# Optimization experiments

Measured on AMD Instinct MI355X. Metric: run time of the kernel, lower is better.

Reference implementation:

```python
import jax, jax.numpy as jnp
import numpy as np

B, L, D, H = 2, 2048, 1024, 16
HD = D // H  # head_dim = 64


def _clin(xr, xi, Wr, br, Wi, bi):
    # (x_r + i x_i)(W_r + i W_i): out_r = fc_r(x_r) - fc_i(x_i); out_i = fc_r(x_i) + fc_i(x_r)
    rr = xr @ Wr.T + br
    ii = xi @ Wi.T + bi
    ri = xi @ Wr.T + br
    ir = xr @ Wi.T + bi
    return rr - ii, ri + ir


def _heads(x):
    # [B, L, D] -> [B, H, L, HD]
    return x.reshape(B, L, H, HD).transpose(0, 2, 1, 3)


def setup_inputs() -> dict:
    key = jax.random.key(0)
    ks = jax.random.split(key, 11)
    inp = {
        "x_r": jax.random.normal(ks[0], (B, L, D), jnp.float32),
        "x_i": jax.random.normal(ks[1], (B, L, D), jnp.float32),
        "attention_mask": jnp.zeros((B, 1, 1, L), jnp.float32),
    }
    names = ["Wq_r", "Wq_i", "Wk_r", "Wk_i", "Wv_r", "Wv_i", "Wo_r", "Wo_i"]
    for n, k in zip(names, ks[2:10]):
        inp[n] = jax.random.normal(k, (D, D), jnp.float32) * 0.02
        inp["b" + n[1:]] = jnp.zeros((D,), jnp.float32)
    return inp


def reference(x_r, x_i, attention_mask,
              Wq_r, bq_r, Wq_i, bq_i,
              Wk_r, bk_r, Wk_i, bk_i,
              Wv_r, bv_r, Wv_i, bv_i,
              Wo_r, bo_r, Wo_i, bo_i):
    qr, qi = _clin(x_r, x_i, Wq_r, bq_r, Wq_i, bq_i)
    kr, ki = _clin(x_r, x_i, Wk_r, bk_r, Wk_i, bk_i)
    vr, vi = _clin(x_r, x_i, Wv_r, bv_r, Wv_i, bv_i)
    q_r, q_i = _heads(qr), _heads(qi)
    k_r, k_i = _heads(kr), _heads(ki)
    v_r, v_i = _heads(vr), _heads(vi)
    # complex QK^T cross terms -> squared-magnitude interference score
    s_real = jnp.einsum('bhqd,bhkd->bhqk', q_r, k_r) + jnp.einsum('bhqd,bhkd->bhqk', q_i, k_i)
    s_imag = jnp.einsum('bhqd,bhkd->bhqk', q_i, k_r) - jnp.einsum('bhqd,bhkd->bhqk', q_r, k_i)
    interference = (s_real * s_real + s_imag * s_imag) / HD + attention_mask
    attn = jax.nn.softmax(interference, axis=-1)
    c_r = jnp.einsum('bhqk,bhkd->bhqd', attn, v_r).transpose(0, 2, 1, 3).reshape(B, L, D)
    c_i = jnp.einsum('bhqk,bhkd->bhqd', attn, v_i).transpose(0, 2, 1, 3).reshape(B, L, D)
    out_r, out_i = _clin(c_r, c_i, Wo_r, bo_r, Wo_i, bo_i)
    return out_r, out_i
```

## Files before the change

kernel.cpp:

```cpp
#include <hip/hip_runtime.h>
#include <hip/hip_bf16.h>

typedef unsigned short u16;
typedef __attribute__((ext_vector_type(8))) short bf16x8;
typedef __attribute__((ext_vector_type(8))) _Float16 f16x8;
typedef __attribute__((ext_vector_type(8))) unsigned short u16x8;
typedef __attribute__((ext_vector_type(4))) float f32x4;

__device__ __forceinline__ u16 f2b(float f) {
  _Float16 h = (_Float16)f;
  return __builtin_bit_cast(u16, h);
}

__device__ __forceinline__ f32x4 mfma16(bf16x8 a, bf16x8 b, f32x4 c) {
  return __builtin_amdgcn_mfma_f32_16x16x32_f16(
      __builtin_bit_cast(f16x8, a), __builtin_bit_cast(f16x8, b), c, 0, 0, 0);
}

#define GLD16(dst, src) __builtin_amdgcn_global_load_lds( \
    (const __attribute__((address_space(1))) void*)(src), \
    (__attribute__((address_space(3))) void*)(dst), 16, 0, 0)

__global__ void pack_x_kernel(u16* __restrict__ A1, const float* __restrict__ xr,
                              const float* __restrict__ xi) {
  const int id = blockIdx.x * 256 + threadIdx.x;
  const size_t k8 = (size_t)id * 8;
  const int n = (int)(k8 >> 11);
  const int kk = (int)(k8 & 2047);
  const float* src = (kk < 1024) ? (xr + (size_t)n * 1024 + kk)
                                 : (xi + (size_t)n * 1024 + (kk - 1024));
  float4 a = *(const float4*)src;
  float4 c = *(const float4*)(src + 4);
  u16x8 o;
  o[0] = f2b(a.x); o[1] = f2b(a.y); o[2] = f2b(a.z); o[3] = f2b(a.w);
  o[4] = f2b(c.x); o[5] = f2b(c.y); o[6] = f2b(c.z); o[7] = f2b(c.w);
  *(u16x8*)(A1 + k8) = o;
}

__global__ void pack_w_kernel(u16* __restrict__ dst, float* __restrict__ biasDst,
                              const float* __restrict__ Wr, const float* __restrict__ Wi,
                              const float* __restrict__ br, const float* __restrict__ bi,
                              int isim) {
  const int row = blockIdx.x;
  const int kk = threadIdx.x * 8;
  const int half = kk >> 10;
  const int kloc = kk & 1023;
  const float* W = (half == 0) ? (isim ? Wi : Wr) : (isim ? Wr : Wi);
  const float sgn = (half == 1 && !isim) ? -1.f : 1.f;
  const float* src = W + (size_t)row * 1024 + kloc;
  float4 a = *(const float4*)src;
  float4 c = *(const float4*)(src + 4);
  u16x8 o;
  o[0] = f2b(sgn * a.x); o[1] = f2b(sgn * a.y); o[2] = f2b(sgn * a.z); o[3] = f2b(sgn * a.w);
  o[4] = f2b(sgn * c.x); o[5] = f2b(sgn * c.y); o[6] = f2b(sgn * c.z); o[7] = f2b(sgn * c.w);
  *(u16x8*)(dst + (size_t)row * 2048 + kk) = o;
  if (threadIdx.x == 0)
    biasDst[row] = isim ? (br[row] + bi[row]) : (br[row] - bi[row]);
}

template<int OUT_F32>
__global__ __launch_bounds__(256) void gemm_bt(const u16* __restrict__ A,
                                               const u16* __restrict__ Bw,
                                               const float* __restrict__ bias,
                                               void* __restrict__ outp) {
  constexpr int K = 2048;
  __shared__ __align__(16) u16 As[128 * 64];
  __shared__ __align__(16) u16 Bs[128 * 64];
  const int tid = threadIdx.x;
  const int w = tid >> 6, l = tid & 63;
  const int l15 = l & 15, lhi = l >> 4;
  const int m0 = blockIdx.y * 128, n0 = blockIdx.x * 128;
  const int wm = w >> 1, wn = w & 1;
  f32x4 acc[4][4] = {};
  for (int kt = 0; kt < K; kt += 64) {
#pragma unroll
    for (int it = 0; it < 4; ++it) {
      const int grp = it * 4 + w;
      const int cl = grp * 64 + l;
      const int r = cl >> 3;
      const int g = (cl & 7) ^ (r & 7);
      GLD16(As + grp * 512, A + (size_t)(m0 + r) * K + kt + g * 8);
      GLD16(Bs + grp * 512, Bw + (size_t)(n0 + r) * K + kt + g * 8);
    }
    __syncthreads();
#pragma unroll
    for (int ks = 0; ks < 2; ++ks) {
      const int c = ks * 4 + lhi;
      bf16x8 af[4], bfr[4];
#pragma unroll
      for (int mf = 0; mf < 4; ++mf) {
        const int r = wm * 64 + mf * 16 + l15;
        af[mf] = *(const bf16x8*)&As[r * 64 + ((c ^ (r & 7)) << 3)];
      }
#pragma unroll
      for (int nf = 0; nf < 4; ++nf) {
        const int r = wn * 64 + nf * 16 + l15;
        bfr[nf] = *(const bf16x8*)&Bs[r * 64 + ((c ^ (r & 7)) << 3)];
      }
#pragma unroll
      for (int mf = 0; mf < 4; ++mf)
#pragma unroll
        for (int nf = 0; nf < 4; ++nf)
          acc[mf][nf] = mfma16(af[mf], bfr[nf], acc[mf][nf]);
    }
    __syncthreads();
  }
#pragma unroll
  for (int nf = 0; nf < 4; ++nf) {
    const int j = n0 + wn * 64 + nf * 16 + l15;
    const float bv = bias[j];
    const size_t obase = (size_t)(j >> 10) * (4096 * 1024) + (j & 1023);
#pragma unroll
    for (int mf = 0; mf < 4; ++mf) {
#pragma unroll
      for (int i = 0; i < 4; ++i) {
        const int row = m0 + wm * 64 + mf * 16 + lhi * 4 + i;
        const float v = acc[mf][nf][i] + bv;
        if constexpr (OUT_F32) ((float*)outp)[obase + (size_t)row * 1024] = v;
        else                   ((u16*)outp)[obase + (size_t)row * 1024] = f2b(v);
      }
    }
  }
}

__global__ void transpose_v_kernel(const u16* __restrict__ v, u16* __restrict__ vt) {
  __shared__ u16 tile[64 * 65];
  const int tt = blockIdx.x, bh = blockIdx.y, ri = blockIdx.z;
  const int b = bh >> 4, h = bh & 15;
  const size_t M1 = (size_t)4096 * 1024;
  const u16* src = v + (size_t)ri * M1;
  u16* dst = vt + (size_t)ri * 32 * 64 * 2048;
  const int t0 = tt * 64;
#pragma unroll
  for (int e = 0; e < 16; ++e) {
    const int id = e * 256 + threadIdx.x;
    const int row = id >> 6, col = id & 63;
    tile[row * 65 + col] = src[(size_t)(b * 2048 + t0 + row) * 1024 + h * 64 + col];
  }
  __syncthreads();
#pragma unroll
  for (int e = 0; e < 16; ++e) {
    const int id = e * 256 + threadIdx.x;
    const int d = id >> 6, tok = id & 63;
    dst[((size_t)bh * 64 + d) * 2048 + t0 + tok] = tile[tok * 65 + d];
  }
}

__global__ __launch_bounds__(256) void attn_kernel(const u16* __restrict__ qkv,
                                                   const u16* __restrict__ vt,
                                                   const float* __restrict__ mask,
                                                   u16* __restrict__ A2) {
  __shared__ __align__(16) u16 Kr[64 * 64];
  __shared__ __align__(16) u16 Ki[64 * 64];
  __shared__ __align__(16) u16 Vr[64 * 64];
  __shared__ __align__(16) u16 Vi[64 * 64];
  __shared__ __align__(16) u16 Pl[4 * 16 * 72];
  const int tid = threadIdx.x, w = tid >> 6, l = tid & 63;
  const int l15 = l & 15, lhi = l >> 4;
  const int q0 = blockIdx.x * 64;
  const int bh = blockIdx.y;
  const int b = bh >> 4, h = bh & 15;
  const size_t M1 = (size_t)4096 * 1024;
  const u16* qr_b = qkv;
  const u16* qi_b = qkv + M1;
  const u16* kr_b = qkv + 2 * M1;
  const u16* ki_b = qkv + 3 * M1;
  const u16* vtr = vt;
  const u16* vti = vt + (size_t)32 * 64 * 2048;

  const size_t qrow = (size_t)(b * 2048 + q0 + w * 16 + l15) * 1024 + h * 64;
  bf16x8 qr[2], qi[2], qrn[2];
#pragma unroll
  for (int ks = 0; ks < 2; ++ks) {
    qr[ks] = *(const bf16x8*)&qr_b[qrow + ks * 32 + lhi * 8];
    qi[ks] = *(const bf16x8*)&qi_b[qrow + ks * 32 + lhi * 8];
    qrn[ks] = qr[ks] ^ (short)0x8000;
  }
  float mrow[4], lrow[4];
  f32x4 o_r[4] = {}, o_i[4] = {};
#pragma unroll
  for (int i = 0; i < 4; ++i) { mrow[i] = -1e30f; lrow[i] = 0.f; }
  u16* Pw = Pl + w * (16 * 72);

  for (int kt = 0; kt < 32; ++kt) {
    const int k0 = kt * 64;
#pragma unroll
    for (int it = 0; it < 2; ++it) {
      const int grp = it * 4 + w;
      const int cl = grp * 64 + l;
      const int r = cl >> 3;
      const int g = (cl & 7) ^ (r & 7);
      const size_t krow = (size_t)(b * 2048 + k0 + r) * 1024 + h * 64 + g * 8;
      const size_t vrow = (size_t)(bh * 64 + r) * 2048 + k0 + g * 8;
      GLD16(Kr + grp * 512, kr_b + krow);
      GLD16(Ki + grp * 512, ki_b + krow);
      GLD16(Vr + grp * 512, vtr + vrow);
      GLD16(Vi + grp * 512, vti + vrow);
    }
    __syncthreads();
    f32x4 sr[4] = {}, si[4] = {};
#pragma unroll
    for (int nf = 0; nf < 4; ++nf) {
      const int krr = nf * 16 + l15;
      const int sw = krr & 7;
#pragma unroll
      for (int ks = 0; ks < 2; ++ks) {
        const int c = ks * 4 + lhi;
        const int off = krr * 64 + ((c ^ sw) << 3);
        bf16x8 kfr = *(const bf16x8*)&Kr[off];
        bf16x8 kfi = *(const bf16x8*)&Ki[off];
        sr[nf] = mfma16(qr[ks], kfr, sr[nf]);
        sr[nf] = mfma16(qi[ks], kfi, sr[nf]);
        si[nf] = mfma16(qi[ks], kfr, si[nf]);
        si[nf] = mfma16(qrn[ks], kfi, si[nf]);
      }
    }
    float t[4][4];
#pragma unroll
    for (int nf = 0; nf < 4; ++nf) {
      const float mk = mask[b * 2048 + k0 + nf * 16 + l15];
#pragma unroll
      for (int i = 0; i < 4; ++i)
        t[nf][i] = (sr[nf][i] * sr[nf][i] + si[nf][i] * si[nf][i]) * 0.015625f + mk;
    }
    float scale[4];
#pragma unroll
    for (int i = 0; i < 4; ++i) {
      float v = fmaxf(fmaxf(t[0][i], t[1][i]), fmaxf(t[2][i], t[3][i]));
      v = fmaxf(v, __shfl_xor(v, 1, 64));
      v = fmaxf(v, __shfl_xor(v, 2, 64));
      v = fmaxf(v, __shfl_xor(v, 4, 64));
      v = fmaxf(v, __shfl_xor(v, 8, 64));
      const float mn = fmaxf(mrow[i], v);
      scale[i] = __expf(mrow[i] - mn);
      mrow[i] = mn;
    }
    float p[4][4], rs[4] = {0.f, 0.f, 0.f, 0.f};
#pragma unroll
    for (int nf = 0; nf < 4; ++nf)
#pragma unroll
      for (int i = 0; i < 4; ++i) {
        p[nf][i] = __expf(t[nf][i] - mrow[i]);
        rs[i] += p[nf][i];
      }
#pragma unroll
    for (int i = 0; i < 4; ++i) {
      float v = rs[i];
      v += __shfl_xor(v, 1, 64);
      v += __shfl_xor(v, 2, 64);
      v += __shfl_xor(v, 4, 64);
      v += __shfl_xor(v, 8, 64);
      lrow[i] = lrow[i] * scale[i] + v;
#pragma unroll
      for (int nf = 0; nf < 4; ++nf) { o_r[nf][i] *= scale[i]; o_i[nf][i] *= scale[i]; }
    }
#pragma unroll
    for (int nf = 0; nf < 4; ++nf)
#pragma unroll
      for (int i = 0; i < 4; ++i)
        Pw[(lhi * 4 + i) * 72 + nf * 16 + l15] = f2b(p[nf][i]);
#pragma unroll
    for (int ks = 0; ks < 2; ++ks) {
      bf16x8 pa = *(const bf16x8*)&Pw[l15 * 72 + ks * 32 + lhi * 8];
      const int c = ks * 4 + lhi;
#pragma unroll
      for (int nf = 0; nf < 4; ++nf) {
        const int vr = nf * 16 + l15;
        const int off = vr * 64 + ((c ^ (vr & 7)) << 3);
        bf16x8 vfr = *(const bf16x8*)&Vr[off];
        bf16x8 vfi = *(const bf16x8*)&Vi[off];
        o_r[nf] = mfma16(pa, vfr, o_r[nf]);
        o_i[nf] = mfma16(pa, vfi, o_i[nf]);
      }
    }
    __syncthreads();
  }
  float inv[4];
#pragma unroll
  for (int i = 0; i < 4; ++i) inv[i] = 1.f / lrow[i];
  const int rowbase = b * 2048 + q0 + w * 16 + lhi * 4;
#pragma unroll
  for (int nf = 0; nf < 4; ++nf) {
    const int col = h * 64 + nf * 16 + l15;
#pragma unroll
    for (int i = 0; i < 4; ++i) {
      const size_t rw = (size_t)(rowbase + i) * 2048;
      A2[rw + col] = f2b(o_r[nf][i] * inv[i]);
      A2[rw + 1024 + col] = f2b(o_i[nf][i] * inv[i]);
    }
  }
}

extern "C" void kernel_launch(void* const* d_in, const int* in_sizes, int n_in,
                              void* d_out, int out_size, void* d_ws, size_t ws_size,
                              hipStream_t stream) {
  (void)in_sizes; (void)n_in; (void)out_size; (void)ws_size;
  const float* x_r  = (const float*)d_in[0];
  const float* x_i  = (const float*)d_in[1];
  const float* mask = (const float*)d_in[2];
  const float* Wq_r = (const float*)d_in[3];
  const float* bq_r = (const float*)d_in[4];
  const float* Wq_i = (const float*)d_in[5];
  const float* bq_i = (const float*)d_in[6];
  const float* Wk_r = (const float*)d_in[7];
  const float* bk_r = (const float*)d_in[8];
  const float* Wk_i = (const float*)d_in[9];
  const float* bk_i = (const float*)d_in[10];
  const float* Wv_r = (const float*)d_in[11];
  const float* bv_r = (const float*)d_in[12];
  const float* Wv_i = (const float*)d_in[13];
  const float* bv_i = (const float*)d_in[14];
  const float* Wo_r = (const float*)d_in[15];
  const float* bo_r = (const float*)d_in[16];
  const float* Wo_i = (const float*)d_in[17];
  const float* bo_i = (const float*)d_in[18];

  char* ws = (char*)d_ws;
  const size_t M1 = (size_t)4096 * 1024;
  u16* A    = (u16*)(ws);
  u16* B1   = (u16*)(ws + (16u << 20));
  u16* vt   = (u16*)(ws + (16u << 20));
  u16* B2   = (u16*)(ws + (32u << 20));
  u16* qkv  = (u16*)(ws + (40u << 20));
  float* bias1 = (float*)(ws + (88u << 20));
  float* bias2 = (float*)(ws + (88u << 20) + (1u << 15));

  pack_x_kernel<<<4096, 256, 0, stream>>>(A, x_r, x_i);
  pack_w_kernel<<<1024, 256, 0, stream>>>(B1 + 0 * (size_t)1024 * 2048, bias1 + 0,    Wq_r, Wq_i, bq_r, bq_i, 0);
  pack_w_kernel<<<1024, 256, 0, stream>>>(B1 + 1 * (size_t)1024 * 2048, bias1 + 1024, Wq_r, Wq_i, bq_r, bq_i, 1);
  pack_w_kernel<<<1024, 256, 0, stream>>>(B1 + 2 * (size_t)1024 * 2048, bias1 + 2048, Wk_r, Wk_i, bk_r, bk_i, 0);
  pack_w_kernel<<<1024, 256, 0, stream>>>(B1 + 3 * (size_t)1024 * 2048, bias1 + 3072, Wk_r, Wk_i, bk_r, bk_i, 1);
  pack_w_kernel<<<1024, 256, 0, stream>>>(B1 + 4 * (size_t)1024 * 2048, bias1 + 4096, Wv_r, Wv_i, bv_r, bv_i, 0);
  pack_w_kernel<<<1024, 256, 0, stream>>>(B1 + 5 * (size_t)1024 * 2048, bias1 + 5120, Wv_r, Wv_i, bv_r, bv_i, 1);

  gemm_bt<0><<<dim3(48, 32), 256, 0, stream>>>(A, B1, bias1, qkv);

  transpose_v_kernel<<<dim3(32, 32, 2), 256, 0, stream>>>(qkv + 4 * M1, vt);
  pack_w_kernel<<<1024, 256, 0, stream>>>(B2,                      bias2,        Wo_r, Wo_i, bo_r, bo_i, 0);
  pack_w_kernel<<<1024, 256, 0, stream>>>(B2 + (size_t)1024 * 2048, bias2 + 1024, Wo_r, Wo_i, bo_r, bo_i, 1);

  attn_kernel<<<dim3(32, 32), 256, 0, stream>>>(qkv, vt, mask, A);

  gemm_bt<1><<<dim3(16, 32), 256, 0, stream>>>(A, B2, bias2, d_out);
}
```

Baseline: 513.4 us.

## Double-buffer K/V tiles with lazy softmax rescale and deferred row-sum reduction

Splits the K/V shared-memory tiles into two buffers so the next tile's global-to-LDS loads are issued while the current tile is computed, which removes one barrier per iteration. The online softmax now rescales the running max and accumulators only when some row's max grows by more than a threshold, instead of on every tile. The per-tile row-sum shuffle reduction is deferred to a single reduction at the end. MFMA sections are also wrapped in s_setprio. The changes double LDS use for K/V, which may lower occupancy, and let exp values grow up to e^8 before rescaling, which risks fp16 range issues in the P tile.

```diff
diff --git a/kernel.cpp b/kernel.cpp
--- a/kernel.cpp
+++ b/kernel.cpp
@@ -150,10 +150,7 @@
                                                    const u16* __restrict__ vt,
                                                    const float* __restrict__ mask,
                                                    u16* __restrict__ A2) {
-  __shared__ __align__(16) u16 Kr[64 * 64];
-  __shared__ __align__(16) u16 Ki[64 * 64];
-  __shared__ __align__(16) u16 Vr[64 * 64];
-  __shared__ __align__(16) u16 Vi[64 * 64];
+  __shared__ __align__(16) u16 KVb[2][4][64 * 64];
   __shared__ __align__(16) u16 Pl[4 * 16 * 72];
   const int tid = threadIdx.x, w = tid >> 6, l = tid & 63;
   const int l15 = l & 15, lhi = l >> 4;
@@ -176,29 +173,41 @@
     qi[ks] = *(const bf16x8*)&qi_b[qrow + ks * 32 + lhi * 8];
     qrn[ks] = qr[ks] ^ (short)0x8000;
   }
-  float mrow[4], lrow[4];
+  float mrow[4], srow[4];
   f32x4 o_r[4] = {}, o_i[4] = {};
 #pragma unroll
-  for (int i = 0; i < 4; ++i) { mrow[i] = -1e30f; lrow[i] = 0.f; }
+  for (int i = 0; i < 4; ++i) { mrow[i] = -1e30f; srow[i] = 0.f; }
   u16* Pw = Pl + w * (16 * 72);
 
-  for (int kt = 0; kt < 32; ++kt) {
-    const int k0 = kt * 64;
+  auto STAGE = [&](int tile, int bufi) {
+    const int k0s = tile * 64;
 #pragma unroll
     for (int it = 0; it < 2; ++it) {
       const int grp = it * 4 + w;
       const int cl = grp * 64 + l;
       const int r = cl >> 3;
       const int g = (cl & 7) ^ (r & 7);
-      const size_t krow = (size_t)(b * 2048 + k0 + r) * 1024 + h * 64 + g * 8;
-      const size_t vrow = (size_t)(bh * 64 + r) * 2048 + k0 + g * 8;
-      GLD16(Kr + grp * 512, kr_b + krow);
-      GLD16(Ki + grp * 512, ki_b + krow);
-      GLD16(Vr + grp * 512, vtr + vrow);
-      GLD16(Vi + grp * 512, vti + vrow);
-    }
+      const size_t krow = (size_t)(b * 2048 + k0s + r) * 1024 + h * 64 + g * 8;
+      const size_t vrow = (size_t)(bh * 64 + r) * 2048 + k0s + g * 8;
+      GLD16(&KVb[bufi][0][grp * 512], kr_b + krow);
+      GLD16(&KVb[bufi][1][grp * 512], ki_b + krow);
+      GLD16(&KVb[bufi][2][grp * 512], vtr + vrow);
+      GLD16(&KVb[bufi][3][grp * 512], vti + vrow);
+    }
+  };
+
+  STAGE(0, 0);
+  for (int kt = 0; kt < 32; ++kt) {
+    const int cur = kt & 1;
+    const int k0 = kt * 64;
     __syncthreads();
+    if (kt < 31) STAGE(kt + 1, cur ^ 1);
+    const u16* Kr = &KVb[cur][0][0];
+    const u16* Ki = &KVb[cur][1][0];
+    const u16* Vr = &KVb[cur][2][0];
+    const u16* Vi = &KVb[cur][3][0];
     f32x4 sr[4] = {}, si[4] = {};
+    __builtin_amdgcn_s_setprio(1);
 #pragma unroll
     for (int nf = 0; nf < 4; ++nf) {
       const int krr = nf * 16 + l15;
@@ -215,6 +224,7 @@
         si[nf] = mfma16(qrn[ks], kfi, si[nf]);
       }
     }
+    __builtin_amdgcn_s_setprio(0);
     float t[4][4];
 #pragma unroll
     for (int nf = 0; nf < 4; ++nf) {
@@ -223,7 +233,7 @@
       for (int i = 0; i < 4; ++i)
         t[nf][i] = (sr[nf][i] * sr[nf][i] + si[nf][i] * si[nf][i]) * 0.015625f + mk;
     }
-    float scale[4];
+    float pmax[4];
 #pragma unroll
     for (int i = 0; i < 4; ++i) {
       float v = fmaxf(fmaxf(t[0][i], t[1][i]), fmaxf(t[2][i], t[3][i]));
@@ -231,34 +241,36 @@
       v = fmaxf(v, __shfl_xor(v, 2, 64));
       v = fmaxf(v, __shfl_xor(v, 4, 64));
       v = fmaxf(v, __shfl_xor(v, 8, 64));
-      const float mn = fmaxf(mrow[i], v);
-      scale[i] = __expf(mrow[i] - mn);
-      mrow[i] = mn;
-    }
-    float p[4][4], rs[4] = {0.f, 0.f, 0.f, 0.f};
+      pmax[i] = v;
+    }
+    bool grow = false;
+#pragma unroll
+    for (int i = 0; i < 4; ++i) grow |= (pmax[i] > mrow[i] + 8.f);
+    if (__any(grow)) {
+#pragma unroll
+      for (int i = 0; i < 4; ++i) {
+        const float mn = fmaxf(mrow[i], pmax[i]);
+        const float sc = __expf(mrow[i] - mn);
+        mrow[i] = mn;
+        srow[i] *= sc;
+#pragma unroll
+        for (int nf = 0; nf < 4; ++nf) { o_r[nf][i] *= sc; o_i[nf][i] *= sc; }
+      }
+    }
+    float p[4][4];
 #pragma unroll
     for (int nf = 0; nf < 4; ++nf)
 #pragma unroll
       for (int i = 0; i < 4; ++i) {
         p[nf][i] = __expf(t[nf][i] - mrow[i]);
-        rs[i] += p[nf][i];
-      }
-#pragma unroll
-    for (int i = 0; i < 4; ++i) {
-      float v = rs[i];
-      v += __shfl_xor(v, 1, 64);
-      v += __shfl_xor(v, 2, 64);
-      v += __shfl_xor(v, 4, 64);
-      v += __shfl_xor(v, 8, 64);
-      lrow[i] = lrow[i] * scale[i] + v;
-#pragma unroll
-      for (int nf = 0; nf < 4; ++nf) { o_r[nf][i] *= scale[i]; o_i[nf][i] *= scale[i]; }
-    }
+        srow[i] += p[nf][i];
+      }
 #pragma unroll
     for (int nf = 0; nf < 4; ++nf)
 #pragma unroll
       for (int i = 0; i < 4; ++i)
         Pw[(lhi * 4 + i) * 72 + nf * 16 + l15] = f2b(p[nf][i]);
+    __builtin_amdgcn_s_setprio(1);
 #pragma unroll
     for (int ks = 0; ks < 2; ++ks) {
       bf16x8 pa = *(const bf16x8*)&Pw[l15 * 72 + ks * 32 + lhi * 8];
@@ -273,11 +285,18 @@
         o_i[nf] = mfma16(pa, vfi, o_i[nf]);
       }
     }
-    __syncthreads();
+    __builtin_amdgcn_s_setprio(0);
   }
   float inv[4];
 #pragma unroll
-  for (int i = 0; i < 4; ++i) inv[i] = 1.f / lrow[i];
+  for (int i = 0; i < 4; ++i) {
+    float v = srow[i];
+    v += __shfl_xor(v, 1, 64);
+    v += __shfl_xor(v, 2, 64);
+    v += __shfl_xor(v, 4, 64);
+    v += __shfl_xor(v, 8, 64);
+    inv[i] = 1.f / v;
+  }
   const int rowbase = b * 2048 + q0 + w * 16 + lhi * 4;
 #pragma unroll
   for (int nf = 0; nf < 4; ++nf) {
```

Measured after the change: 478.2 us. 6.8% less time.
